# Kernel tuning notes

Hardware: AMD Instinct MI355X
Metric: run time of the kernel (lower is better)

Reference implementation:

```python
import jax, jax.numpy as jnp
import numpy as np

V, D, NE, K, C = 500000, 128, 1000000, 8, 16
H1 = 8  # 2**l with l=3


def setup_inputs() -> dict:
    key = jax.random.key(0)
    ks = jax.random.split(key, 12)
    def w(k, shape, fan_in):
        return jax.random.normal(k, shape, jnp.float32) / np.sqrt(fan_in)
    return {
        "X": jax.random.normal(ks[0], (V, D), jnp.float32),
        "E": jax.random.randint(ks[1], (NE, K), 0, V, jnp.int64),
        "rv": jax.random.uniform(ks[2], (D,), jnp.float32),
        "W1": w(ks[3], (D, H1), D), "b1": jnp.zeros((H1,), jnp.float32),
        "W2": w(ks[4], (H1, H1), H1), "b2": jnp.zeros((H1,), jnp.float32),
        "W3": w(ks[5], (H1, C), H1), "b3": jnp.zeros((C,), jnp.float32),
        "fc_w": w(ks[6], (C, 1), C), "fc_b": jnp.zeros((1,), jnp.float32),
    }


def build_laplacian(X, E, rv):
    """HyperGCN fast Laplacian (no mediators): per hyperedge pick the
    argmax/argmin nodes of a random projection, connect them symmetrically
    with weight 1/|e|, add identity, symmetric D^-1/2 normalization.
    Returns (rows, cols, vals, diag_vals) of the sparse normalized adjacency."""
    n, k = X.shape[0], E.shape[1]
    proj = X @ rv                      # [V]
    p = proj[E]                        # [NE, K]
    ar = jnp.arange(E.shape[0])
    Se = E[ar, jnp.argmax(p, axis=1)]  # [NE]
    Ie = E[ar, jnp.argmin(p, axis=1)]  # [NE]
    rows = jnp.concatenate([Se, Ie])
    cols = jnp.concatenate([Ie, Se])
    vals = jnp.full(rows.shape, 1.0 / k, dtype=X.dtype)
    deg = jnp.ones((n,), X.dtype).at[rows].add(vals)  # +1 from identity
    dinv = jax.lax.rsqrt(deg)
    vals_n = vals * dinv[rows] * dinv[cols]
    diag_vals = dinv * dinv
    return rows, cols, vals_n, diag_vals


def spmm(rows, cols, vals, diag_vals, M):
    # (A_norm + normalized identity) @ M, M: [V, F]
    out = diag_vals[:, None] * M
    return out.at[rows].add(vals[:, None] * M[cols])


def reference(X, E, rv, W1, b1, W2, b2, W3, b3, fc_w, fc_b):
    rows, cols, vals, dvals = build_laplacian(X, E, rv)
    # dropout p=0.1 is a no-op in eval mode
    H = jax.nn.relu(spmm(rows, cols, vals, dvals, X @ W1) + b1)
    H = jax.nn.relu(spmm(rows, cols, vals, dvals, H @ W2) + b2)
    H = jax.nn.relu(spmm(rows, cols, vals, dvals, H @ W3) + b3)
    logits = (H @ fc_w + fc_b)[:, 0]   # [V]
    return jax.nn.sigmoid(logits)
```

## Files before the change

### kernel.cpp

```cpp
#include <hip/hip_runtime.h>
#include <hip/hip_bf16.h>

static constexpr int VN = 500000;
static constexpr int DD = 128;
static constexpr int NE = 1000000;
static constexpr int KE = 8;
static constexpr int CC = 16;
static constexpr int H1 = 8;
static constexpr int EW = 64;
static constexpr int TR = 64;
static constexpr int LSTR = 129;

typedef float fvec4 __attribute__((ext_vector_type(4)));
typedef int   ivec4 __attribute__((ext_vector_type(4)));

__global__ __launch_bounds__(64) void k_row(const float* __restrict__ X,
                                            const float* __restrict__ rv,
                                            const float* __restrict__ W1,
                                            float* __restrict__ proj,
                                            float* __restrict__ A,
                                            int* __restrict__ fill) {
    __shared__ float xs[TR * LSTR];
    int v0 = blockIdx.x * TR;
    int tid = threadIdx.x;
    int nrows = min(TR, VN - v0);
    int totalF4 = nrows * (DD / 4);
    const float4* X4 = reinterpret_cast<const float4*>(X) + (size_t)v0 * (DD / 4);
#pragma unroll 4
    for (int i = tid; i < totalF4; i += 64) {
        float4 t = X4[i];
        int r = i >> 5;
        int c = (i & 31) << 2;
        float* dst = &xs[r * LSTR + c];
        dst[0] = t.x; dst[1] = t.y; dst[2] = t.z; dst[3] = t.w;
    }
    __syncthreads();
    int v = v0 + tid;
    if (tid >= nrows || v >= VN) return;
    float accP = 0.f;
    float accM[H1];
#pragma unroll
    for (int j = 0; j < H1; ++j) accM[j] = 0.f;
    const float* xrow = &xs[tid * LSTR];
#pragma unroll 8
    for (int j = 0; j < DD; ++j) {
        float x = xrow[j];
        accP += x * rv[j];
        const float4* wr = reinterpret_cast<const float4*>(W1 + (size_t)j * H1);
        float4 wa = wr[0], wb = wr[1];
        accM[0] += x * wa.x; accM[1] += x * wa.y;
        accM[2] += x * wa.z; accM[3] += x * wa.w;
        accM[4] += x * wb.x; accM[5] += x * wb.y;
        accM[6] += x * wb.z; accM[7] += x * wb.w;
    }
    proj[v] = accP;
    fill[v] = 0;
    float4* a4 = reinterpret_cast<float4*>(A + (size_t)v * H1);
    a4[0] = make_float4(accM[0], accM[1], accM[2], accM[3]);
    a4[1] = make_float4(accM[4], accM[5], accM[6], accM[7]);
}

__global__ __launch_bounds__(256) void k_place(const int* __restrict__ E,
                                               const float* __restrict__ proj,
                                               int* __restrict__ fill,
                                               int* __restrict__ ell) {
    int e = blockIdx.x * 256 + threadIdx.x;
    if (e >= NE) return;
    const ivec4* er = reinterpret_cast<const ivec4*>(E + (size_t)e * KE);
    ivec4 e0 = __builtin_nontemporal_load(&er[0]);
    ivec4 e1 = __builtin_nontemporal_load(&er[1]);
    int ids[KE] = {e0.x, e0.y, e0.z, e0.w, e1.x, e1.y, e1.z, e1.w};
    float p[KE];
#pragma unroll
    for (int j = 0; j < KE; ++j) p[j] = proj[ids[j]];
    float bestMax = p[0], bestMin = p[0];
    int idMax = ids[0], idMin = ids[0];
#pragma unroll
    for (int j = 1; j < KE; ++j) {
        if (p[j] > bestMax) { bestMax = p[j]; idMax = ids[j]; }
        if (p[j] < bestMin) { bestMin = p[j]; idMin = ids[j]; }
    }
    int ps = atomicAdd(fill + idMax, 1);
    int pi = atomicAdd(fill + idMin, 1);
    if (ps < EW) __builtin_nontemporal_store(idMin, ell + (size_t)idMax * EW + ps);
    if (pi < EW) __builtin_nontemporal_store(idMax, ell + (size_t)idMin * EW + pi);
}

template <int FIN, int FOUT, int RSI, int RSO, bool PRE>
__global__ __launch_bounds__(256) void k_glayer(const int* __restrict__ ell,
                                                const int* __restrict__ fill,
                                                const float* __restrict__ bias,
                                                const float* __restrict__ W,
                                                const float* __restrict__ Min,
                                                float* __restrict__ Mout) {
    int v = blockIdx.x * 256 + threadIdx.x;
    if (v >= VN) return;
    int deg = fill[v];
    float di = rsqrtf(1.0f + 0.125f * (float)deg);
    deg = min(deg, EW);
    float s[FIN];
#pragma unroll
    for (int j = 0; j < FIN; ++j) s[j] = 0.f;
    const int* row = ell + (size_t)v * EW;
    int p = 0;
    for (; p + 4 <= deg; p += 4) {
        int4 c4 = *reinterpret_cast<const int4*>(row + p);
        float sc0 = 1.f, sc1 = 1.f, sc2 = 1.f, sc3 = 1.f;
        if (!PRE) {
            sc0 = rsqrtf(1.0f + 0.125f * (float)fill[c4.x]);
            sc1 = rsqrtf(1.0f + 0.125f * (float)fill[c4.y]);
            sc2 = rsqrtf(1.0f + 0.125f * (float)fill[c4.z]);
            sc3 = rsqrtf(1.0f + 0.125f * (float)fill[c4.w]);
        }
        const float4* r0 = reinterpret_cast<const float4*>(Min + (size_t)c4.x * RSI);
        const float4* r1 = reinterpret_cast<const float4*>(Min + (size_t)c4.y * RSI);
        const float4* r2 = reinterpret_cast<const float4*>(Min + (size_t)c4.z * RSI);
        const float4* r3 = reinterpret_cast<const float4*>(Min + (size_t)c4.w * RSI);
        float4 t0[FIN / 4], t1[FIN / 4], t2[FIN / 4], t3[FIN / 4];
#pragma unroll
        for (int j = 0; j < FIN / 4; ++j) t0[j] = r0[j];
#pragma unroll
        for (int j = 0; j < FIN / 4; ++j) t1[j] = r1[j];
#pragma unroll
        for (int j = 0; j < FIN / 4; ++j) t2[j] = r2[j];
#pragma unroll
        for (int j = 0; j < FIN / 4; ++j) t3[j] = r3[j];
#pragma unroll
        for (int j = 0; j < FIN / 4; ++j) {
            s[4 * j]     += sc0 * t0[j].x + sc1 * t1[j].x + sc2 * t2[j].x + sc3 * t3[j].x;
            s[4 * j + 1] += sc0 * t0[j].y + sc1 * t1[j].y + sc2 * t2[j].y + sc3 * t3[j].y;
            s[4 * j + 2] += sc0 * t0[j].z + sc1 * t1[j].z + sc2 * t2[j].z + sc3 * t3[j].z;
            s[4 * j + 3] += sc0 * t0[j].w + sc1 * t1[j].w + sc2 * t2[j].w + sc3 * t3[j].w;
        }
    }
    for (; p < deg; ++p) {
        int c = row[p];
        float sc = 1.f;
        if (!PRE) sc = rsqrtf(1.0f + 0.125f * (float)fill[c]);
        const float4* cr = reinterpret_cast<const float4*>(Min + (size_t)c * RSI);
#pragma unroll
        for (int j = 0; j < FIN / 4; ++j) {
            float4 t = cr[j];
            s[4 * j] += sc * t.x; s[4 * j + 1] += sc * t.y;
            s[4 * j + 2] += sc * t.z; s[4 * j + 3] += sc * t.w;
        }
    }
    const float4* mr = reinterpret_cast<const float4*>(Min + (size_t)v * RSI);
    float own[FIN];
#pragma unroll
    for (int j = 0; j < FIN / 4; ++j) {
        float4 t = mr[j];
        own[4 * j] = t.x; own[4 * j + 1] = t.y;
        own[4 * j + 2] = t.z; own[4 * j + 3] = t.w;
    }
    float osc = PRE ? 1.0f : di;
    float h[FIN];
#pragma unroll
    for (int j = 0; j < FIN; ++j) {
        float y = di * (osc * own[j] + 0.125f * s[j]) + bias[j];
        h[j] = y > 0.f ? y : 0.f;
    }
#pragma unroll
    for (int c = 0; c < FOUT; ++c) {
        float m = 0.f;
#pragma unroll
        for (int j = 0; j < FIN; ++j) m += h[j] * W[j * FOUT + c];
        Mout[(size_t)v * RSO + c] = di * m;
    }
}

__global__ __launch_bounds__(256) void k_gfinal(const int* __restrict__ ell,
                                                const int* __restrict__ fill,
                                                const float* __restrict__ b3,
                                                const float* __restrict__ fcw,
                                                const float* __restrict__ fcb,
                                                const float* __restrict__ Min,
                                                float* __restrict__ out) {
    int v = blockIdx.x * 256 + threadIdx.x;
    if (v >= VN) return;
    int deg = fill[v];
    float di = rsqrtf(1.0f + 0.125f * (float)deg);
    deg = min(deg, EW);
    float s[CC];
#pragma unroll
    for (int j = 0; j < CC; ++j) s[j] = 0.f;
    const int* row = ell + (size_t)v * EW;
    int p = 0;
    for (; p + 2 <= deg; p += 2) {
        int c0 = row[p], c1 = row[p + 1];
        const float4* r0 = reinterpret_cast<const float4*>(Min + (size_t)c0 * CC);
        const float4* r1 = reinterpret_cast<const float4*>(Min + (size_t)c1 * CC);
        float4 t0[CC / 4], t1[CC / 4];
#pragma unroll
        for (int j = 0; j < CC / 4; ++j) t0[j] = r0[j];
#pragma unroll
        for (int j = 0; j < CC / 4; ++j) t1[j] = r1[j];
#pragma unroll
        for (int j = 0; j < CC / 4; ++j) {
            s[4 * j]     += t0[j].x + t1[j].x;
            s[4 * j + 1] += t0[j].y + t1[j].y;
            s[4 * j + 2] += t0[j].z + t1[j].z;
            s[4 * j + 3] += t0[j].w + t1[j].w;
        }
    }
    if (p < deg) {
        int c = row[p];
        const float4* cr = reinterpret_cast<const float4*>(Min + (size_t)c * CC);
#pragma unroll
        for (int j = 0; j < CC / 4; ++j) {
            float4 t = cr[j];
            s[4 * j] += t.x; s[4 * j + 1] += t.y;
            s[4 * j + 2] += t.z; s[4 * j + 3] += t.w;
        }
    }
    const float4* mr = reinterpret_cast<const float4*>(Min + (size_t)v * CC);
    float own[CC];
#pragma unroll
    for (int j = 0; j < CC / 4; ++j) {
        float4 t = mr[j];
        own[4 * j] = t.x; own[4 * j + 1] = t.y;
        own[4 * j + 2] = t.z; own[4 * j + 3] = t.w;
    }
    float acc = fcb[0];
#pragma unroll
    for (int j = 0; j < CC; ++j) {
        float y = di * (own[j] + 0.125f * s[j]) + b3[j];
        float hh = y > 0.f ? y : 0.f;
        acc += hh * fcw[j];
    }
    out[v] = 1.f / (1.f + expf(-acc));
}

extern "C" void kernel_launch(void* const* d_in, const int* in_sizes, int n_in,
                              void* d_out, int out_size, void* d_ws, size_t ws_size,
                              hipStream_t stream) {
    const float* X   = (const float*)d_in[0];
    const int*   E   = (const int*)d_in[1];
    const float* rv  = (const float*)d_in[2];
    const float* W1  = (const float*)d_in[3];
    const float* b1  = (const float*)d_in[4];
    const float* W2  = (const float*)d_in[5];
    const float* b2  = (const float*)d_in[6];
    const float* W3  = (const float*)d_in[7];
    const float* b3  = (const float*)d_in[8];
    const float* fcw = (const float*)d_in[9];
    const float* fcb = (const float*)d_in[10];
    float* out = (float*)d_out;

    float* ws = (float*)d_ws;
    float* A    = ws;
    float* B    = ws + 4000000;
    float* C    = ws + 8000000;
    float* proj = ws + 16000000;
    int*   fill = (int*)(ws + 16500000);
    int*   ell  = (int*)(ws + 17000000);

    dim3 blkR(64), blk(256);
    int gR = (VN + TR - 1) / TR;
    int gV = (VN + 255) / 256;
    int gE = (NE + 255) / 256;

    k_row<<<gR, blkR, 0, stream>>>(X, rv, W1, proj, A, fill);
    k_place<<<gE, blk, 0, stream>>>(E, proj, fill, ell);

    k_glayer<8, 8, 8, 8, false><<<gV, blk, 0, stream>>>(ell, fill, b1, W2, A, B);
    k_glayer<8, 16, 8, 16, true><<<gV, blk, 0, stream>>>(ell, fill, b2, W3, B, C);
    k_gfinal<<<gV, blk, 0, stream>>>(ell, fill, b3, fcw, fcb, C, out);
}
```

Measured before the change: 359.2 us.

## Sort vertices into degree buckets and pre-scale features to remove neighbor degree lookups

```diff
diff --git a/kernel.cpp b/kernel.cpp
--- a/kernel.cpp
+++ b/kernel.cpp
@@ -10,6 +10,7 @@
 static constexpr int EW = 64;
 static constexpr int TR = 64;
 static constexpr int LSTR = 129;
+static constexpr int NBK = 64;
 
 typedef float fvec4 __attribute__((ext_vector_type(4)));
 typedef int   ivec4 __attribute__((ext_vector_type(4)));
@@ -19,14 +20,15 @@
                                             const float* __restrict__ W1,
                                             float* __restrict__ proj,
                                             float* __restrict__ A,
-                                            int* __restrict__ fill) {
+                                            int* __restrict__ fill,
+                                            int* __restrict__ gcnt) {
     __shared__ float xs[TR * LSTR];
     int v0 = blockIdx.x * TR;
     int tid = threadIdx.x;
     int nrows = min(TR, VN - v0);
     int totalF4 = nrows * (DD / 4);
     const float4* X4 = reinterpret_cast<const float4*>(X) + (size_t)v0 * (DD / 4);
-#pragma unroll 4
+#pragma unroll 8
     for (int i = tid; i < totalF4; i += 64) {
         float4 t = X4[i];
         int r = i >> 5;
@@ -37,6 +39,7 @@
     __syncthreads();
     int v = v0 + tid;
     if (tid >= nrows || v >= VN) return;
+    if (v < NBK) gcnt[v] = 0;
     float accP = 0.f;
     float accM[H1];
 #pragma unroll
@@ -86,18 +89,75 @@
     if (pi < EW) __builtin_nontemporal_store(idMax, ell + (size_t)idMin * EW + pi);
 }
 
-template <int FIN, int FOUT, int RSI, int RSO, bool PRE>
-__global__ __launch_bounds__(256) void k_glayer(const int* __restrict__ ell,
-                                                const int* __restrict__ fill,
+__global__ __launch_bounds__(256) void k_prep(const int* __restrict__ fill,
+                                              float* __restrict__ A,
+                                              int* __restrict__ gcnt) {
+    __shared__ int hist[NBK];
+    if (threadIdx.x < NBK) hist[threadIdx.x] = 0;
+    __syncthreads();
+    int v = blockIdx.x * 256 + threadIdx.x;
+    if (v < VN) {
+        int deg = fill[v];
+        float di = rsqrtf(1.0f + 0.125f * (float)deg);
+        float4* ar = reinterpret_cast<float4*>(A + (size_t)v * H1);
+        float4 a0 = ar[0], a1 = ar[1];
+        ar[0] = make_float4(di * a0.x, di * a0.y, di * a0.z, di * a0.w);
+        ar[1] = make_float4(di * a1.x, di * a1.y, di * a1.z, di * a1.w);
+        atomicAdd(&hist[min(deg, NBK - 1)], 1);
+    }
+    __syncthreads();
+    if (threadIdx.x < NBK && hist[threadIdx.x] > 0)
+        atomicAdd(&gcnt[threadIdx.x], hist[threadIdx.x]);
+}
+
+__global__ __launch_bounds__(64) void k_scanb(const int* __restrict__ gcnt,
+                                              int* __restrict__ cursor) {
+    int l = threadIdx.x;
+    int d = NBK - 1 - l;
+    int val = gcnt[d];
+    int orig = val;
+#pragma unroll
+    for (int off = 1; off < 64; off <<= 1) {
+        int n = __shfl_up(val, off);
+        if (l >= off) val += n;
+    }
+    cursor[d] = val - orig;
+}
+
+__global__ __launch_bounds__(256) void k_scatter(const int* __restrict__ fill,
+                                                 int* __restrict__ cursor,
+                                                 int* __restrict__ perm) {
+    __shared__ int hist[NBK];
+    __shared__ int base[NBK];
+    if (threadIdx.x < NBK) hist[threadIdx.x] = 0;
+    __syncthreads();
+    int v = blockIdx.x * 256 + threadIdx.x;
+    int b = 0, local = 0;
+    if (v < VN) {
+        b = min(fill[v], NBK - 1);
+        local = atomicAdd(&hist[b], 1);
+    }
+    __syncthreads();
+    if (threadIdx.x < NBK)
+        base[threadIdx.x] = hist[threadIdx.x] > 0
+            ? atomicAdd(&cursor[threadIdx.x], hist[threadIdx.x]) : 0;
+    __syncthreads();
+    if (v < VN) perm[base[b] + local] = (v << 6) | b;
+}
+
+template <int FIN, int FOUT, int RSI, int RSO>
+__global__ __launch_bounds__(256) void k_glayer(const int* __restrict__ perm,
+                                                const int* __restrict__ ell,
                                                 const float* __restrict__ bias,
                                                 const float* __restrict__ W,
                                                 const float* __restrict__ Min,
                                                 float* __restrict__ Mout) {
-    int v = blockIdx.x * 256 + threadIdx.x;
-    if (v >= VN) return;
-    int deg = fill[v];
+    int t = blockIdx.x * 256 + threadIdx.x;
+    if (t >= VN) return;
+    int packed = perm[t];
+    int v = packed >> 6;
+    int deg = packed & 63;
     float di = rsqrtf(1.0f + 0.125f * (float)deg);
-    deg = min(deg, EW);
     float s[FIN];
 #pragma unroll
     for (int j = 0; j < FIN; ++j) s[j] = 0.f;
@@ -105,13 +165,6 @@
     int p = 0;
     for (; p + 4 <= deg; p += 4) {
         int4 c4 = *reinterpret_cast<const int4*>(row + p);
-        float sc0 = 1.f, sc1 = 1.f, sc2 = 1.f, sc3 = 1.f;
-        if (!PRE) {
-            sc0 = rsqrtf(1.0f + 0.125f * (float)fill[c4.x]);
-            sc1 = rsqrtf(1.0f + 0.125f * (float)fill[c4.y]);
-            sc2 = rsqrtf(1.0f + 0.125f * (float)fill[c4.z]);
-            sc3 = rsqrtf(1.0f + 0.125f * (float)fill[c4.w]);
-        }
         const float4* r0 = reinterpret_cast<const float4*>(Min + (size_t)c4.x * RSI);
         const float4* r1 = reinterpret_cast<const float4*>(Min + (size_t)c4.y * RSI);
         const float4* r2 = reinterpret_cast<const float4*>(Min + (size_t)c4.z * RSI);
@@ -127,37 +180,34 @@
         for (int j = 0; j < FIN / 4; ++j) t3[j] = r3[j];
 #pragma unroll
         for (int j = 0; j < FIN / 4; ++j) {
-            s[4 * j]     += sc0 * t0[j].x + sc1 * t1[j].x + sc2 * t2[j].x + sc3 * t3[j].x;
-            s[4 * j + 1] += sc0 * t0[j].y + sc1 * t1[j].y + sc2 * t2[j].y + sc3 * t3[j].y;
-            s[4 * j + 2] += sc0 * t0[j].z + sc1 * t1[j].z + sc2 * t2[j].z + sc3 * t3[j].z;
-            s[4 * j + 3] += sc0 * t0[j].w + sc1 * t1[j].w + sc2 * t2[j].w + sc3 * t3[j].w;
+            s[4 * j]     += t0[j].x + t1[j].x + t2[j].x + t3[j].x;
+            s[4 * j + 1] += t0[j].y + t1[j].y + t2[j].y + t3[j].y;
+            s[4 * j + 2] += t0[j].z + t1[j].z + t2[j].z + t3[j].z;
+            s[4 * j + 3] += t0[j].w + t1[j].w + t2[j].w + t3[j].w;
         }
     }
     for (; p < deg; ++p) {
         int c = row[p];
-        float sc = 1.f;
-        if (!PRE) sc = rsqrtf(1.0f + 0.125f * (float)fill[c]);
         const float4* cr = reinterpret_cast<const float4*>(Min + (size_t)c * RSI);
 #pragma unroll
         for (int j = 0; j < FIN / 4; ++j) {
-            float4 t = cr[j];
-            s[4 * j] += sc * t.x; s[4 * j + 1] += sc * t.y;
-            s[4 * j + 2] += sc * t.z; s[4 * j + 3] += sc * t.w;
+            float4 tt = cr[j];
+            s[4 * j] += tt.x; s[4 * j + 1] += tt.y;
+            s[4 * j + 2] += tt.z; s[4 * j + 3] += tt.w;
         }
     }
     const float4* mr = reinterpret_cast<const float4*>(Min + (size_t)v * RSI);
     float own[FIN];
 #pragma unroll
     for (int j = 0; j < FIN / 4; ++j) {
-        float4 t = mr[j];
-        own[4 * j] = t.x; own[4 * j + 1] = t.y;
-        own[4 * j + 2] = t.z; own[4 * j + 3] = t.w;
-    }
-    float osc = PRE ? 1.0f : di;
+        float4 tt = mr[j];
+        own[4 * j] = tt.x; own[4 * j + 1] = tt.y;
+        own[4 * j + 2] = tt.z; own[4 * j + 3] = tt.w;
+    }
     float h[FIN];
 #pragma unroll
     for (int j = 0; j < FIN; ++j) {
-        float y = di * (osc * own[j] + 0.125f * s[j]) + bias[j];
+        float y = di * (own[j] + 0.125f * s[j]) + bias[j];
         h[j] = y > 0.f ? y : 0.f;
     }
 #pragma unroll
@@ -169,18 +219,19 @@
     }
 }
 
-__global__ __launch_bounds__(256) void k_gfinal(const int* __restrict__ ell,
-                                                const int* __restrict__ fill,
+__global__ __launch_bounds__(256) void k_gfinal(const int* __restrict__ perm,
+                                                const int* __restrict__ ell,
                                                 const float* __restrict__ b3,
                                                 const float* __restrict__ fcw,
                                                 const float* __restrict__ fcb,
                                                 const float* __restrict__ Min,
                                                 float* __restrict__ out) {
-    int v = blockIdx.x * 256 + threadIdx.x;
-    if (v >= VN) return;
-    int deg = fill[v];
+    int t = blockIdx.x * 256 + threadIdx.x;
+    if (t >= VN) return;
+    int packed = perm[t];
+    int v = packed >> 6;
+    int deg = packed & 63;
     float di = rsqrtf(1.0f + 0.125f * (float)deg);
-    deg = min(deg, EW);
     float s[CC];
 #pragma unroll
     for (int j = 0; j < CC; ++j) s[j] = 0.f;
@@ -208,18 +259,18 @@
         const float4* cr = reinterpret_cast<const float4*>(Min + (size_t)c * CC);
 #pragma unroll
         for (int j = 0; j < CC / 4; ++j) {
-            float4 t = cr[j];
-            s[4 * j] += t.x; s[4 * j + 1] += t.y;
-            s[4 * j + 2] += t.z; s[4 * j + 3] += t.w;
+            float4 tt = cr[j];
+            s[4 * j] += tt.x; s[4 * j + 1] += tt.y;
+            s[4 * j + 2] += tt.z; s[4 * j + 3] += tt.w;
         }
     }
     const float4* mr = reinterpret_cast<const float4*>(Min + (size_t)v * CC);
     float own[CC];
 #pragma unroll
     for (int j = 0; j < CC / 4; ++j) {
-        float4 t = mr[j];
-        own[4 * j] = t.x; own[4 * j + 1] = t.y;
-        own[4 * j + 2] = t.z; own[4 * j + 3] = t.w;
+        float4 tt = mr[j];
+        own[4 * j] = tt.x; own[4 * j + 1] = tt.y;
+        own[4 * j + 2] = tt.z; own[4 * j + 3] = tt.w;
     }
     float acc = fcb[0];
 #pragma unroll
@@ -248,22 +299,28 @@
     float* out = (float*)d_out;
 
     float* ws = (float*)d_ws;
-    float* A    = ws;
-    float* B    = ws + 4000000;
-    float* C    = ws + 8000000;
-    float* proj = ws + 16000000;
-    int*   fill = (int*)(ws + 16500000);
-    int*   ell  = (int*)(ws + 17000000);
+    float* A      = ws;
+    float* B      = ws + 4000000;
+    float* C      = ws + 8000000;
+    float* proj   = ws + 16000000;
+    int*   fill   = (int*)(ws + 16500000);
+    int*   perm   = (int*)(ws + 17000000);
+    int*   gcnt   = (int*)(ws + 17500000);
+    int*   cursor = (int*)(ws + 17500128);
+    int*   ell    = (int*)(ws + 18000000);
 
     dim3 blkR(64), blk(256);
     int gR = (VN + TR - 1) / TR;
     int gV = (VN + 255) / 256;
     int gE = (NE + 255) / 256;
 
-    k_row<<<gR, blkR, 0, stream>>>(X, rv, W1, proj, A, fill);
+    k_row<<<gR, blkR, 0, stream>>>(X, rv, W1, proj, A, fill, gcnt);
     k_place<<<gE, blk, 0, stream>>>(E, proj, fill, ell);
-
-    k_glayer<8, 8, 8, 8, false><<<gV, blk, 0, stream>>>(ell, fill, b1, W2, A, B);
-    k_glayer<8, 16, 8, 16, true><<<gV, blk, 0, stream>>>(ell, fill, b2, W3, B, C);
-    k_gfinal<<<gV, blk, 0, stream>>>(ell, fill, b3, fcw, fcb, C, out);
-}
+    k_prep<<<gV, blk, 0, stream>>>(fill, A, gcnt);
+    k_scanb<<<1, blkR, 0, stream>>>(gcnt, cursor);
+    k_scatter<<<gV, blk, 0, stream>>>(fill, cursor, perm);
+
+    k_glayer<8, 8, 8, 8><<<gV, blk, 0, stream>>>(perm, ell, b1, W2, A, B);
+    k_glayer<8, 16, 8, 16><<<gV, blk, 0, stream>>>(perm, ell, b2, W3, B, C);
+    k_gfinal<<<gV, blk, 0, stream>>>(perm, ell, b3, fcw, fcb, C, out);
+}
```

New measurement: 434.0 us. 20.8% more time.
